# Kernel tuning notes

Measured on AMD Instinct MI355X. Metric: run time of the kernel, lower is better.

## Reference

```python
import jax, jax.numpy as jnp
import numpy as np
import math

ALPHA_MIN = math.exp(-1.0 / 5.0)   # ~0.8187
ALPHA_MAX = math.exp(-1.0 / 25.0)  # ~0.9608
THRESHOLD = 1.0


def setup_inputs() -> dict:
    key = jax.random.key(0)
    k1, k2, k3, k4, k5 = jax.random.split(key, 5)
    B, T, I, H = 32, 2048, 256, 512
    x = jax.random.normal(k1, (B, T, I), dtype=jnp.float32)
    # Linear weight, kaiming-ish scale
    W = jax.random.normal(k2, (H, I), dtype=jnp.float32) * (1.0 / np.sqrt(I))
    # alpha ~ U[exp(-1/5), exp(-1/25)] as in nn.init.uniform_
    alpha = ALPHA_MIN + jax.random.uniform(k3, (H,), dtype=jnp.float32) * (ALPHA_MAX - ALPHA_MIN)
    # initial membrane potential / spike state (torch.rand in _lif_cell)
    u0 = jax.random.uniform(k4, (B, H), dtype=jnp.float32)
    s0 = jax.random.uniform(k5, (B, H), dtype=jnp.float32)
    return {"x": x, "W": W, "alpha": alpha, "u0": u0, "s0": s0}


def reference(x, W, alpha, u0, s0):
    # clamp alpha to its admissible range (lif_feature has no 'NoClamp')
    alpha = jnp.clip(alpha, ALPHA_MIN, ALPHA_MAX)
    b = 1.0 - alpha  # lif_feature has no 'B'

    # feedforward projection: [B, T, H]
    Wx = jnp.einsum('bti,hi->bth', x, W)

    def step(carry, wx_t):
        ut, st = carry
        ut = alpha * (ut - st) + b * wx_t          # leaky integrate + soft reset
        st = (ut - THRESHOLD > 0).astype(ut.dtype)  # heaviside spike
        return (ut, st), st

    # scan over time: Wx -> [T, B, H]
    _, s = jax.lax.scan(step, (u0, s0), jnp.swapaxes(Wx, 0, 1))
    return jnp.swapaxes(s, 0, 1)  # [B, T, H]
```

## Files before the change

### kernel.cpp

```cpp
#include <hip/hip_runtime.h>

#define ALPHA_MIN 0.8187307530779818f
#define ALPHA_MAX 0.9607894391523232f

typedef _Float16 f16;
typedef _Float16 f16x4 __attribute__((ext_vector_type(4)));
typedef _Float16 f16x8 __attribute__((ext_vector_type(8)));
typedef float f32x16 __attribute__((ext_vector_type(16)));

#define BB_ 32
#define TT_ 2048
#define KK_ 256
#define HH_ 512
#define TC_ 64
#define NC_ 32
#define KH_ 128

__device__ __forceinline__ void barrier_lds() {
    __builtin_amdgcn_s_waitcnt(0xC07F);
    __builtin_amdgcn_s_barrier();
}

__global__ __launch_bounds__(320, 1) void lif_fused4(
    const float* __restrict__ X,
    const float* __restrict__ W,
    const float* __restrict__ alpha,
    const float* __restrict__ u0,
    const float* __restrict__ s0,
    float* __restrict__ out)
{
    __shared__ f16 Ah[TC_ * KH_];
    __shared__ f16 Al[TC_ * KH_];
    __shared__ float wxbuf[2][TC_ * 64];

    const int b  = blockIdx.x & 31;
    const int nt = blockIdx.x >> 5;
    const int n0 = nt * 64;

    const int tid  = threadIdx.x;
    const int wv   = tid >> 6;
    const int lane = tid & 63;
    const int fm   = lane & 31;
    const int fq   = lane >> 5;

    if (wv < 4) {
        const int mh = wv >> 1;
        const int nh = wv & 1;

        f16x8 bh[16], bl[16];
        {
            const float* wp = W + (size_t)(n0 + nh * 32 + fm) * KK_ + fq * 8;
#pragma unroll
            for (int ks = 0; ks < 16; ++ks) {
                float4 v0 = *(const float4*)(wp + ks * 16);
                float4 v1 = *(const float4*)(wp + ks * 16 + 4);
                float v[8] = {v0.x, v0.y, v0.z, v0.w, v1.x, v1.y, v1.z, v1.w};
                f16x8 h, l;
#pragma unroll
                for (int j = 0; j < 8; ++j) {
                    const f16 hj = (f16)v[j];
                    h[j] = hj;
                    l[j] = (f16)((v[j] - (float)hj) * 2048.0f);
                }
                bh[ks] = h; bl[ks] = l;
            }
        }

        f32x16 accH, accLa, accLb;
#pragma unroll
        for (int e = 0; e < 16; ++e) { accH[e] = 0.0f; accLa[e] = 0.0f; accLb[e] = 0.0f; }

        const int srow_j = wv * 16 + (lane >> 5);
        const int f4i    = lane & 31;
        const int g      = f4i >> 1;
        const int sub    = f4i & 1;

        float4 pend[8];
        auto issue_loads = [&](int c, int kh) {
            const float* base = X + ((size_t)b * TT_ + c * TC_) * KK_ + kh * KH_ + f4i * 4;
#pragma unroll
            for (int j = 0; j < 8; ++j)
                pend[j] = *(const float4*)(base + (size_t)(srow_j + j * 2) * KK_);
        };
        auto cvt_write = [&]() {
#pragma unroll
            for (int j = 0; j < 8; ++j) {
                const int row = srow_j + j * 2;
                const float v[4] = {pend[j].x, pend[j].y, pend[j].z, pend[j].w};
                f16x4 h, l;
#pragma unroll
                for (int e = 0; e < 4; ++e) {
                    const f16 he = (f16)v[e];
                    h[e] = he;
                    l[e] = (f16)((v[e] - (float)he) * 2048.0f);
                }
                const int addr = row * KH_ + ((g ^ (row & 15)) * 8) + sub * 4;
                *(f16x4*)&Ah[addr] = h;
                *(f16x4*)&Al[addr] = l;
            }
        };
        auto compute_half = [&](int hf) {
            const int row = mh * 32 + fm;
            const int r15 = row & 15;
#pragma unroll
            for (int ks = 0; ks < 8; ++ks) {
                const int addr = row * KH_ + (((ks * 2 + fq) ^ r15) * 8);
                const f16x8 ah = *(const f16x8*)&Ah[addr];
                const f16x8 al = *(const f16x8*)&Al[addr];
                const int ksg = hf * 8 + ks;
                accH  = __builtin_amdgcn_mfma_f32_32x32x16_f16(ah, bh[ksg], accH,  0, 0, 0);
                accLa = __builtin_amdgcn_mfma_f32_32x32x16_f16(ah, bl[ksg], accLa, 0, 0, 0);
                accLb = __builtin_amdgcn_mfma_f32_32x32x16_f16(al, bh[ksg], accLb, 0, 0, 0);
            }
        };

        issue_loads(0, 0);

        for (int c = 0; c < NC_; ++c) {
            cvt_write();
            issue_loads(c, 1);
            barrier_lds();
            compute_half(0);
            barrier_lds();
            cvt_write();
            if (c + 1 < NC_) issue_loads(c + 1, 0);
            barrier_lds();
            compute_half(1);
            {
                float* wb = &wxbuf[c & 1][0];
                const int colw = nh * 32 + fm;
#pragma unroll
                for (int r = 0; r < 16; ++r) {
                    const int roww = mh * 32 + (r & 3) + 8 * (r >> 2) + 4 * fq;
                    wb[roww * 64 + colw] = accH[r] + (accLa[r] + accLb[r]) * (1.0f / 2048.0f);
                    accH[r] = 0.0f; accLa[r] = 0.0f; accLb[r] = 0.0f;
                }
            }
            barrier_lds();
        }
    } else {
        const int h = n0 + lane;
        const int chain = b * HH_ + h;
        float a = alpha[h];
        a = fminf(fmaxf(a, ALPHA_MIN), ALPHA_MAX);
        const float bbv = 1.0f - a;
        float u = u0[chain];
        float s = s0[chain];
        float* op = out + (size_t)b * TT_ * HH_ + h;

        auto consume = [&](int c, int hf) {
            const float* wb = &wxbuf[c & 1][0];
            const int tb = c * TC_ + hf * 32;
#pragma unroll
            for (int t0 = 0; t0 < 32; t0 += 8) {
                float w[8];
#pragma unroll
                for (int j = 0; j < 8; ++j) w[j] = wb[(hf * 32 + t0 + j) * 64 + lane];
#pragma unroll
                for (int j = 0; j < 8; ++j) {
                    u = fmaf(a, u - s, bbv * w[j]);
                    s = (u > 1.0f) ? 1.0f : 0.0f;
                    __builtin_nontemporal_store(s, &op[(size_t)(tb + t0 + j) * HH_]);
                }
            }
        };

        for (int c = 0; c < NC_; ++c) {
            barrier_lds();
            if (c > 0) consume(c - 1, 0);
            barrier_lds();
            barrier_lds();
            if (c > 0) consume(c - 1, 1);
            barrier_lds();
        }
        consume(NC_ - 1, 0);
        consume(NC_ - 1, 1);
    }
}

__global__ void gemm_naive(const float* __restrict__ X, const float* __restrict__ W,
                           float* __restrict__ C, int M, int N, int K)
{
    const int idx = blockIdx.x * 256 + threadIdx.x;
    if (idx >= M * N) return;
    const int m = idx / N, n = idx % N;
    float acc = 0.0f;
    for (int k = 0; k < K; ++k) acc = fmaf(X[(size_t)m * K + k], W[(size_t)n * K + k], acc);
    C[idx] = acc;
}

__global__ __launch_bounds__(64) void lif_scan_inplace(
    float* __restrict__ buf, const float* __restrict__ alpha,
    const float* __restrict__ u0, const float* __restrict__ s0, int T, int H)
{
    const int chain = blockIdx.x * 64 + threadIdx.x;
    const int h = chain % H;
    const int b = chain / H;
    float a = alpha[h];
    a = fminf(fmaxf(a, ALPHA_MIN), ALPHA_MAX);
    const float bb = 1.0f - a;
    float u = u0[chain], s = s0[chain];
    float* base = buf + (size_t)b * T * H + h;
    for (int t = 0; t < T; ++t) {
        u = fmaf(a, u - s, bb * base[(size_t)t * H]);
        s = (u > 1.0f) ? 1.0f : 0.0f;
        base[(size_t)t * H] = s;
    }
}

extern "C" void kernel_launch(void* const* d_in, const int* in_sizes, int n_in,
                              void* d_out, int out_size, void* d_ws, size_t ws_size,
                              hipStream_t stream) {
    const float* x     = (const float*)d_in[0];
    const float* W     = (const float*)d_in[1];
    const float* alpha = (const float*)d_in[2];
    const float* u0    = (const float*)d_in[3];
    const float* s0    = (const float*)d_in[4];
    float* out = (float*)d_out;

    const int H = in_sizes[2];
    const int I = in_sizes[1] / H;
    const int B = in_sizes[3] / H;
    const int T = in_sizes[0] / (B * I);

    if (B == BB_ && T == TT_ && I == KK_ && H == HH_) {
        lif_fused4<<<256, 320, 0, stream>>>(x, W, alpha, u0, s0, out);
    } else {
        const int M = B * T;
        gemm_naive<<<(M * H + 255) / 256, 256, 0, stream>>>(x, W, out, M, H, I);
        lif_scan_inplace<<<(B * H + 63) / 64, 64, 0, stream>>>(out, alpha, u0, s0, T, H);
    }
}
```

Measured before the change: 280.6 us.

## Use direct global-to-LDS async loads with triple buffering and narrower N tiles

The fused GEMM+scan kernel now streams X tiles straight into LDS as fp32 with global_load_lds in a three-deep ring, and converts to split fp16 at read time instead of staging through registers. The N tile shrinks from 64 to 32 columns, giving 512 blocks of 192 threads with two blocks per CU, and the barrier count per chunk drops. The aim is better overlap of memory loads with MFMA and scan work and higher occupancy. The cost is that each X tile is now read twice as often across N tiles, conversion work is repeated per MFMA wave, and half the scan wave's lanes sit idle.

```diff
diff --git a/kernel.cpp b/kernel.cpp
--- a/kernel.cpp
+++ b/kernel.cpp
@@ -4,7 +4,6 @@
 #define ALPHA_MAX 0.9607894391523232f
 
 typedef _Float16 f16;
-typedef _Float16 f16x4 __attribute__((ext_vector_type(4)));
 typedef _Float16 f16x8 __attribute__((ext_vector_type(8)));
 typedef float f32x16 __attribute__((ext_vector_type(16)));
 
@@ -14,14 +13,32 @@
 #define HH_ 512
 #define TC_ 64
 #define NC_ 32
-#define KH_ 128
+#define NB_ 32
+#define KQ_ 64
+
+__device__ __forceinline__ void gll16(const float* g, float* l) {
+    __builtin_amdgcn_global_load_lds(
+        (const __attribute__((address_space(1))) void*)g,
+        (__attribute__((address_space(3))) void*)l, 16, 0, 0);
+}
 
 __device__ __forceinline__ void barrier_lds() {
     __builtin_amdgcn_s_waitcnt(0xC07F);
     __builtin_amdgcn_s_barrier();
 }
 
-__global__ __launch_bounds__(320, 1) void lif_fused4(
+__device__ __forceinline__ void cvt8(const float4 v0, const float4 v1,
+                                     f16x8& h, f16x8& l) {
+    const float v[8] = {v0.x, v0.y, v0.z, v0.w, v1.x, v1.y, v1.z, v1.w};
+#pragma unroll
+    for (int j = 0; j < 8; ++j) {
+        const f16 hj = (f16)v[j];
+        h[j] = hj;
+        l[j] = (f16)((v[j] - (float)hj) * 2048.0f);
+    }
+}
+
+__global__ __launch_bounds__(192, 2) void lif_fused5(
     const float* __restrict__ X,
     const float* __restrict__ W,
     const float* __restrict__ alpha,
@@ -29,13 +46,12 @@
     const float* __restrict__ s0,
     float* __restrict__ out)
 {
-    __shared__ f16 Ah[TC_ * KH_];
-    __shared__ f16 Al[TC_ * KH_];
-    __shared__ float wxbuf[2][TC_ * 64];
+    __shared__ float Abuf[3][TC_ * KQ_];
+    __shared__ float wxbuf[2][TC_ * NB_];
 
     const int b  = blockIdx.x & 31;
     const int nt = blockIdx.x >> 5;
-    const int n0 = nt * 64;
+    const int n0 = nt * NB_;
 
     const int tid  = threadIdx.x;
     const int wv   = tid >> 6;
@@ -43,103 +59,83 @@
     const int fm   = lane & 31;
     const int fq   = lane >> 5;
 
-    if (wv < 4) {
-        const int mh = wv >> 1;
-        const int nh = wv & 1;
+    if (wv < 2) {
+        const int mh  = wv;
+        const int rlo = lane >> 4;
+        const int sl  = lane & 15;
+
+        const float* xb = X + (size_t)b * TT_ * KK_;
+
+        auto issue_q = [&](int q) {
+            const int c = q >> 2, kq = q & 3, bf = q % 3;
+#pragma unroll
+            for (int j = 0; j < 8; ++j) {
+                const int r0  = mh * 32 + j * 4;
+                const int row = r0 + rlo;
+                const int g   = sl ^ (row & 15);
+                gll16(xb + (size_t)(c * TC_ + row) * KK_ + kq * KQ_ + g * 4,
+                      &Abuf[bf][r0 * KQ_]);
+            }
+        };
+        issue_q(0);
+        issue_q(1);
 
         f16x8 bh[16], bl[16];
         {
-            const float* wp = W + (size_t)(n0 + nh * 32 + fm) * KK_ + fq * 8;
+            const float* wp = W + (size_t)(n0 + fm) * KK_ + fq * 8;
 #pragma unroll
             for (int ks = 0; ks < 16; ++ks) {
                 float4 v0 = *(const float4*)(wp + ks * 16);
                 float4 v1 = *(const float4*)(wp + ks * 16 + 4);
-                float v[8] = {v0.x, v0.y, v0.z, v0.w, v1.x, v1.y, v1.z, v1.w};
-                f16x8 h, l;
-#pragma unroll
-                for (int j = 0; j < 8; ++j) {
-                    const f16 hj = (f16)v[j];
-                    h[j] = hj;
-                    l[j] = (f16)((v[j] - (float)hj) * 2048.0f);
+                cvt8(v0, v1, bh[ks], bl[ks]);
+            }
+        }
+
+        f32x16 accH, accLa, accLb;
+#pragma unroll
+        for (int e = 0; e < 16; ++e) { accH[e] = 0.0f; accLa[e] = 0.0f; accLb[e] = 0.0f; }
+
+        const int row = mh * 32 + fm;
+        const int r15 = row & 15;
+
+        for (int c = 0; c < NC_; ++c) {
+            barrier_lds();
+#pragma unroll
+            for (int kq = 0; kq < 4; ++kq) {
+                if (c < NC_ - 1 || kq < 2)
+                    __builtin_amdgcn_s_waitcnt(0x0F78);
+                else
+                    __builtin_amdgcn_s_waitcnt(0x0F70);
+                __builtin_amdgcn_sched_barrier(0);
+
+                const int q  = c * 4 + kq;
+                const float* ab = &Abuf[q % 3][row * KQ_];
+#pragma unroll
+                for (int ks = 0; ks < 4; ++ks) {
+                    const int G  = ks * 4 + fq * 2;
+                    const float4 a0 = *(const float4*)&ab[((G    ) ^ r15) * 4];
+                    const float4 a1 = *(const float4*)&ab[((G + 1) ^ r15) * 4];
+                    f16x8 ah, al;
+                    cvt8(a0, a1, ah, al);
+                    const int ksg = kq * 4 + ks;
+                    accH  = __builtin_amdgcn_mfma_f32_32x32x16_f16(ah, bh[ksg], accH,  0, 0, 0);
+                    accLa = __builtin_amdgcn_mfma_f32_32x32x16_f16(ah, bl[ksg], accLa, 0, 0, 0);
+                    accLb = __builtin_amdgcn_mfma_f32_32x32x16_f16(al, bh[ksg], accLb, 0, 0, 0);
                 }
-                bh[ks] = h; bl[ks] = l;
+                if (q + 2 < NC_ * 4) issue_q(q + 2);
+            }
+            float* wb = &wxbuf[c & 1][0];
+#pragma unroll
+            for (int r = 0; r < 16; ++r) {
+                const int roww = mh * 32 + (r & 3) + 8 * (r >> 2) + 4 * fq;
+                wb[roww * NB_ + fm] = accH[r] + (accLa[r] + accLb[r]) * (1.0f / 2048.0f);
+                accH[r] = 0.0f; accLa[r] = 0.0f; accLb[r] = 0.0f;
             }
         }
-
-        f32x16 accH, accLa, accLb;
-#pragma unroll
-        for (int e = 0; e < 16; ++e) { accH[e] = 0.0f; accLa[e] = 0.0f; accLb[e] = 0.0f; }
-
-        const int srow_j = wv * 16 + (lane >> 5);
-        const int f4i    = lane & 31;
-        const int g      = f4i >> 1;
-        const int sub    = f4i & 1;
-
-        float4 pend[8];
-        auto issue_loads = [&](int c, int kh) {
-            const float* base = X + ((size_t)b * TT_ + c * TC_) * KK_ + kh * KH_ + f4i * 4;
-#pragma unroll
-            for (int j = 0; j < 8; ++j)
-                pend[j] = *(const float4*)(base + (size_t)(srow_j + j * 2) * KK_);
-        };
-        auto cvt_write = [&]() {
-#pragma unroll
-            for (int j = 0; j < 8; ++j) {
-                const int row = srow_j + j * 2;
-                const float v[4] = {pend[j].x, pend[j].y, pend[j].z, pend[j].w};
-                f16x4 h, l;
-#pragma unroll
-                for (int e = 0; e < 4; ++e) {
-                    const f16 he = (f16)v[e];
-                    h[e] = he;
-                    l[e] = (f16)((v[e] - (float)he) * 2048.0f);
-                }
-                const int addr = row * KH_ + ((g ^ (row & 15)) * 8) + sub * 4;
-                *(f16x4*)&Ah[addr] = h;
-                *(f16x4*)&Al[addr] = l;
-            }
-        };
-        auto compute_half = [&](int hf) {
-            const int row = mh * 32 + fm;
-            const int r15 = row & 15;
-#pragma unroll
-            for (int ks = 0; ks < 8; ++ks) {
-                const int addr = row * KH_ + (((ks * 2 + fq) ^ r15) * 8);
-                const f16x8 ah = *(const f16x8*)&Ah[addr];
-                const f16x8 al = *(const f16x8*)&Al[addr];
-                const int ksg = hf * 8 + ks;
-                accH  = __builtin_amdgcn_mfma_f32_32x32x16_f16(ah, bh[ksg], accH,  0, 0, 0);
-                accLa = __builtin_amdgcn_mfma_f32_32x32x16_f16(ah, bl[ksg], accLa, 0, 0, 0);
-                accLb = __builtin_amdgcn_mfma_f32_32x32x16_f16(al, bh[ksg], accLb, 0, 0, 0);
-            }
-        };
-
-        issue_loads(0, 0);
-
-        for (int c = 0; c < NC_; ++c) {
-            cvt_write();
-            issue_loads(c, 1);
-            barrier_lds();
-            compute_half(0);
-            barrier_lds();
-            cvt_write();
-            if (c + 1 < NC_) issue_loads(c + 1, 0);
-            barrier_lds();
-            compute_half(1);
-            {
-                float* wb = &wxbuf[c & 1][0];
-                const int colw = nh * 32 + fm;
-#pragma unroll
-                for (int r = 0; r < 16; ++r) {
-                    const int roww = mh * 32 + (r & 3) + 8 * (r >> 2) + 4 * fq;
-                    wb[roww * 64 + colw] = accH[r] + (accLa[r] + accLb[r]) * (1.0f / 2048.0f);
-                    accH[r] = 0.0f; accLa[r] = 0.0f; accLb[r] = 0.0f;
-                }
-            }
-            barrier_lds();
-        }
+        barrier_lds();
     } else {
-        const int h = n0 + lane;
+        const int hl = lane & 31;
+        const int h  = n0 + hl;
         const int chain = b * HH_ + h;
         float a = alpha[h];
         a = fminf(fmaxf(a, ALPHA_MIN), ALPHA_MAX);
@@ -147,34 +143,31 @@
         float u = u0[chain];
         float s = s0[chain];
         float* op = out + (size_t)b * TT_ * HH_ + h;
-
-        auto consume = [&](int c, int hf) {
-            const float* wb = &wxbuf[c & 1][0];
-            const int tb = c * TC_ + hf * 32;
-#pragma unroll
-            for (int t0 = 0; t0 < 32; t0 += 8) {
+        const bool writer = (lane < 32);
+
+        auto consume = [&](int cc) {
+            const float* wb = &wxbuf[cc & 1][0];
+            const int tb = cc * TC_;
+            for (int t0 = 0; t0 < TC_; t0 += 8) {
                 float w[8];
 #pragma unroll
-                for (int j = 0; j < 8; ++j) w[j] = wb[(hf * 32 + t0 + j) * 64 + lane];
+                for (int j = 0; j < 8; ++j) w[j] = wb[(t0 + j) * NB_ + hl];
 #pragma unroll
                 for (int j = 0; j < 8; ++j) {
                     u = fmaf(a, u - s, bbv * w[j]);
                     s = (u > 1.0f) ? 1.0f : 0.0f;
-                    __builtin_nontemporal_store(s, &op[(size_t)(tb + t0 + j) * HH_]);
+                    if (writer)
+                        __builtin_nontemporal_store(s, &op[(size_t)(tb + t0 + j) * HH_]);
                 }
             }
         };
 
         for (int c = 0; c < NC_; ++c) {
             barrier_lds();
-            if (c > 0) consume(c - 1, 0);
-            barrier_lds();
-            barrier_lds();
-            if (c > 0) consume(c - 1, 1);
-            barrier_lds();
+            if (c > 0) consume(c - 1);
         }
-        consume(NC_ - 1, 0);
-        consume(NC_ - 1, 1);
+        barrier_lds();
+        consume(NC_ - 1);
     }
 }
 
@@ -224,7 +217,7 @@
     const int T = in_sizes[0] / (B * I);
 
     if (B == BB_ && T == TT_ && I == KK_ && H == HH_) {
-        lif_fused4<<<256, 320, 0, stream>>>(x, W, alpha, u0, s0, out);
+        lif_fused5<<<512, 192, 0, stream>>>(x, W, alpha, u0, s0, out);
     } else {
         const int M = B * T;
         gemm_naive<<<(M * H + 255) / 256, 256, 0, stream>>>(x, W, out, M, H, I);
```

After: 440.9 us. +57.1%, slower.
